# Kernel tuning notes

Measured on AMD Instinct MI355X. Metric: run time of the kernel, lower is better.

The kernel has to match this reference:

```python
import jax, jax.numpy as jnp
import numpy as np

HEADS = 8
DIM_HEAD = 64
SCALE = DIM_HEAD ** -0.5


def setup_inputs() -> dict:
    key = jax.random.key(0)
    k1, k2, k3, k4 = jax.random.split(key, 4)
    b, n, dim = 4, 1024, 512
    inner = HEADS * DIM_HEAD  # 512
    x = jax.random.normal(k1, (b, n, dim), dtype=jnp.float32)
    spd = jax.random.normal(k2, (b, HEADS, n, n), dtype=jnp.float32)
    head_keep = jnp.ones((HEADS,), dtype=jnp.float32)  # deterministic stand-in for binomial head drop
    w_qkv = jax.random.normal(k3, (dim, 3 * inner), dtype=jnp.float32) * (dim ** -0.5)
    w_out = jax.random.normal(k4, (inner, dim), dtype=jnp.float32) * (inner ** -0.5)
    b_out = jnp.zeros((dim,), dtype=jnp.float32)
    return {"x": x, "spd": spd, "head_keep": head_keep, "w_qkv": w_qkv, "w_out": w_out, "b_out": b_out}


def reference(x, spd, head_keep, w_qkv, w_out, b_out):
    b, n, dim = x.shape
    qkv = x @ w_qkv  # [b, n, 3*inner]
    q, k, v = jnp.split(qkv, 3, axis=-1)

    def to_heads(t):  # [b, n, h*d] -> [b, h, n, d]
        return t.reshape(b, n, HEADS, DIM_HEAD).transpose(0, 2, 1, 3)

    q, k, v = to_heads(q), to_heads(k), to_heads(v)
    dots = jnp.einsum('bhid,bhjd->bhij', q, k) * SCALE + spd  # [b, h, n, n]
    attn = jax.nn.softmax(dots, axis=-1)
    # random head drop + rescale: attn * mask * H / sum(keep)
    keep_sum = jnp.sum(head_keep)
    attn = attn * (head_keep[None, :, None, None] * (HEADS / keep_sum))
    out = jnp.einsum('bhij,bhjd->bhid', attn, v)  # [b, h, n, d]
    out = out.transpose(0, 2, 1, 3).reshape(b, n, HEADS * DIM_HEAD)
    return out @ w_out + b_out
```

## Files before the change

### kernel.cpp

```cpp
#include <hip/hip_runtime.h>
#include <math.h>

#define NSEQ   1024
#define HEADS  8
#define DHEAD  64
#define SCALE  0.125f
#define LOG2E  1.4426950408889634f

typedef unsigned int u32;
typedef unsigned short u16;
typedef short short8 __attribute__((ext_vector_type(8)));
typedef __bf16 bf16x2 __attribute__((ext_vector_type(2)));
typedef __bf16 bf16x8 __attribute__((ext_vector_type(8)));
typedef float f32x4  __attribute__((ext_vector_type(4)));
typedef float f32x16 __attribute__((ext_vector_type(16)));

__device__ __forceinline__ u16 f2bf(float f) {
    __bf16 h = (__bf16)f;
    return __builtin_bit_cast(u16, h);
}
__device__ __forceinline__ u32 pk2(float lo, float hi) {
    bf16x2 v; v[0] = (__bf16)lo; v[1] = (__bf16)hi;
    return __builtin_bit_cast(u32, v);
}
__device__ __forceinline__ short8 cvt8(float4 a, float4 b) {
    bf16x8 v;
    v[0] = (__bf16)a.x; v[1] = (__bf16)a.y; v[2] = (__bf16)a.z; v[3] = (__bf16)a.w;
    v[4] = (__bf16)b.x; v[5] = (__bf16)b.y; v[6] = (__bf16)b.z; v[7] = (__bf16)b.w;
    return __builtin_bit_cast(short8, v);
}
__device__ __forceinline__ float exp2_fast(float x) {
#if __has_builtin(__builtin_amdgcn_exp2f)
    return __builtin_amdgcn_exp2f(x);
#else
    return exp2f(x);
#endif
}
__device__ __forceinline__ f32x4 mfma16(short8 a, short8 b, f32x4 c) {
    return __builtin_amdgcn_mfma_f32_16x16x32_bf16(a, b, c, 0, 0, 0);
}
__device__ __forceinline__ f32x16 mfma32(short8 a, short8 b, f32x16 c) {
    return __builtin_amdgcn_mfma_f32_32x32x16_bf16(a, b, c, 0, 0, 0);
}

__global__ __launch_bounds__(256) void prep(const float* __restrict__ wqkv,
                                            const float* __restrict__ wout,
                                            u16* __restrict__ wqkvT,
                                            u16* __restrict__ woutT) {
    __shared__ float T[64][65];
    const int t = threadIdx.x;
    const int bb = blockIdx.x;
    const float* in; u16* outp; int K, N, n0, k0;
    if (bb < 192) {
        in = wqkv; outp = wqkvT; K = 512; N = 1536;
        n0 = (bb % 24) * 64; k0 = (bb / 24) * 64;
    } else {
        int bid = bb - 192;
        in = wout; outp = woutT; K = 512; N = 512;
        n0 = (bid % 8) * 64; k0 = (bid / 8) * 64;
    }
    #pragma unroll
    for (int rep = 0; rep < 4; ++rep) {
        int r = rep * 16 + (t >> 4), c = (t & 15) * 4;
        float4 v = *(const float4*)&in[(size_t)(k0 + r) * N + n0 + c];
        T[r][c + 0] = v.x; T[r][c + 1] = v.y; T[r][c + 2] = v.z; T[r][c + 3] = v.w;
    }
    __syncthreads();
    const int nl = t >> 2, kb = (t & 3) * 16;
    bf16x8 s0, s1;
    #pragma unroll
    for (int e = 0; e < 8; ++e) s0[e] = (__bf16)T[kb + e][nl];
    #pragma unroll
    for (int e = 0; e < 8; ++e) s1[e] = (__bf16)T[kb + 8 + e][nl];
    *(short8*)&outp[(size_t)(n0 + nl) * K + k0 + kb]     = __builtin_bit_cast(short8, s0);
    *(short8*)&outp[(size_t)(n0 + nl) * K + k0 + kb + 8] = __builtin_bit_cast(short8, s1);
}

__global__ __launch_bounds__(256) void gemm_qkv_mfma(const float* __restrict__ x,
                                                     const u16* __restrict__ wT,
                                                     u16* __restrict__ qb,
                                                     u16* __restrict__ kb,
                                                     u16* __restrict__ vT) {
    __shared__ u16 As[128][72];
    __shared__ u16 Bs[64][72];
    const int t = threadIdx.x, lane = t & 63, w = t >> 6;
    const int wm = w >> 1, wn = w & 1;
    const int l15 = lane & 15, l4 = lane >> 4;
    const int bid = blockIdx.x;
    const int swz = (bid & 7) * 96 + (bid >> 3);
    const int j0 = (swz % 24) * 64, i0 = (swz / 24) * 128;
    const int which = j0 / 512;
    const int b = i0 >> 10;

    f32x4 acc[8];
    #pragma unroll
    for (int i = 0; i < 8; ++i) acc[i] = (f32x4){0.f, 0.f, 0.f, 0.f};

    const int arow0 = t >> 2, c16 = (t & 3) * 16;

    float4 rax[8];
    short8 rb2[2];
    #pragma unroll
    for (int rep = 0; rep < 2; ++rep)
        #pragma unroll
        for (int q = 0; q < 4; ++q)
            rax[rep * 4 + q] = *(const float4*)&x[(size_t)(i0 + rep * 64 + arow0) * 512 + c16 + q * 4];
    #pragma unroll
    for (int q = 0; q < 2; ++q)
        rb2[q] = *(const short8*)&wT[(size_t)(j0 + arow0) * 512 + c16 + q * 8];

    for (int kt = 0; kt < 8; ++kt) {
        __syncthreads();
        #pragma unroll
        for (int rep = 0; rep < 2; ++rep) {
            *(short8*)&As[rep * 64 + arow0][c16]     = cvt8(rax[rep * 4 + 0], rax[rep * 4 + 1]);
            *(short8*)&As[rep * 64 + arow0][c16 + 8] = cvt8(rax[rep * 4 + 2], rax[rep * 4 + 3]);
        }
        *(short8*)&Bs[arow0][c16]     = rb2[0];
        *(short8*)&Bs[arow0][c16 + 8] = rb2[1];
        __syncthreads();
        if (kt < 7) {
            int k0 = (kt + 1) * 64;
            #pragma unroll
            for (int rep = 0; rep < 2; ++rep)
                #pragma unroll
                for (int q = 0; q < 4; ++q)
                    rax[rep * 4 + q] = *(const float4*)&x[(size_t)(i0 + rep * 64 + arow0) * 512 + k0 + c16 + q * 4];
            #pragma unroll
            for (int q = 0; q < 2; ++q)
                rb2[q] = *(const short8*)&wT[(size_t)(j0 + arow0) * 512 + k0 + c16 + q * 8];
        }
        #pragma unroll
        for (int ks = 0; ks < 2; ++ks) {
            if (which < 2) {
                short8 af[4], bf[2];
                #pragma unroll
                for (int m = 0; m < 4; ++m)
                    af[m] = *(const short8*)&As[wm * 64 + m * 16 + l15][ks * 32 + l4 * 8];
                #pragma unroll
                for (int n = 0; n < 2; ++n)
                    bf[n] = *(const short8*)&Bs[wn * 32 + n * 16 + l15][ks * 32 + l4 * 8];
                #pragma unroll
                for (int m = 0; m < 4; ++m)
                    #pragma unroll
                    for (int n = 0; n < 2; ++n)
                        acc[m * 2 + n] = mfma16(af[m], bf[n], acc[m * 2 + n]);
            } else {
                short8 af[2], bf[4];
                #pragma unroll
                for (int mj = 0; mj < 2; ++mj)
                    af[mj] = *(const short8*)&Bs[wn * 32 + mj * 16 + l15][ks * 32 + l4 * 8];
                #pragma unroll
                for (int ni = 0; ni < 4; ++ni)
                    bf[ni] = *(const short8*)&As[wm * 64 + ni * 16 + l15][ks * 32 + l4 * 8];
                #pragma unroll
                for (int mj = 0; mj < 2; ++mj)
                    #pragma unroll
                    for (int ni = 0; ni < 4; ++ni)
                        acc[mj * 4 + ni] = mfma16(af[mj], bf[ni], acc[mj * 4 + ni]);
            }
        }
    }

    if (which < 2) {
        u16* dst = (which == 0) ? qb : kb;
        const int h = (j0 & 511) >> 6;
        #pragma unroll
        for (int m = 0; m < 4; ++m)
            #pragma unroll
            for (int n = 0; n < 2; ++n) {
                int d = wn * 32 + n * 16 + l15;
                #pragma unroll
                for (int r = 0; r < 4; ++r) {
                    int tok = i0 + wm * 64 + m * 16 + l4 * 4 + r;
                    dst[(((size_t)(b * HEADS + h)) * NSEQ + (tok & 1023)) * DHEAD + d] =
                        f2bf(acc[m * 2 + n][r]);
                }
            }
    } else {
        const int h = (j0 - 1024) >> 6;
        #pragma unroll
        for (int mj = 0; mj < 2; ++mj)
            #pragma unroll
            for (int ni = 0; ni < 4; ++ni) {
                int tok = i0 + wm * 64 + ni * 16 + l15;
                #pragma unroll
                for (int r = 0; r < 4; ++r) {
                    int d = wn * 32 + mj * 16 + l4 * 4 + r;
                    vT[(((size_t)(b * HEADS + h)) * DHEAD + d) * NSEQ + (tok & 1023)] =
                        f2bf(acc[mj * 4 + ni][r]);
                }
            }
    }
}

__global__ __launch_bounds__(256) void attn_mfma(const u16* __restrict__ qb,
                                                 const u16* __restrict__ kb,
                                                 const u16* __restrict__ vT,
                                                 const float* __restrict__ spd,
                                                 const float* __restrict__ head_keep,
                                                 u16* __restrict__ ab) {
    __shared__ u16 Qs[128][72];
    __shared__ u16 Ks[64][72];
    __shared__ u16 Vs[64][72];
    __shared__ float Ss[128][65];

    const int t = threadIdx.x, lane = t & 63, w = t >> 6;
    const int hi = lane >> 5, li = lane & 31;
    const int bh = blockIdx.y, b = bh >> 3, h = bh & 7;
    const int i0 = blockIdx.x * 128;

    const u16* qh = qb + (size_t)bh * NSEQ * DHEAD;
    const u16* kh = kb + (size_t)bh * NSEQ * DHEAD;
    const u16* vh = vT + (size_t)bh * DHEAD * NSEQ;
    const float* sp = spd + (size_t)bh * NSEQ * NSEQ;

    #pragma unroll
    for (int rep = 0; rep < 4; ++rep) {
        int row = rep * 32 + (t >> 3), c8 = (t & 7) * 8;
        *(short8*)&Qs[row][c8] = *(const short8*)&qh[(size_t)(i0 + row) * DHEAD + c8];
    }

    float m_s = -1e30f, l_s = 0.f;
    f32x16 o0 = {}, o1 = {};
    #pragma unroll
    for (int r = 0; r < 16; ++r) { o0[r] = 0.f; o1[r] = 0.f; }

    short8 rk[2], rv[2];
    float4 rs[8];
    {
        int row = t >> 3, c8 = (t & 7) * 8;
        #pragma unroll
        for (int rep = 0; rep < 2; ++rep) {
            rk[rep] = *(const short8*)&kh[(size_t)(rep * 32 + row) * DHEAD + c8];
            rv[rep] = *(const short8*)&vh[(size_t)(rep * 32 + row) * NSEQ + c8];
        }
        #pragma unroll
        for (int rep = 0; rep < 8; ++rep) {
            int rrow = rep * 16 + (t >> 4), c = (t & 15) * 4;
            rs[rep] = *(const float4*)&sp[(size_t)(i0 + rrow) * NSEQ + c];
        }
    }

    for (int jt = 0; jt < 16; ++jt) {
        __syncthreads();
        {
            int row = t >> 3, c8 = (t & 7) * 8;
            #pragma unroll
            for (int rep = 0; rep < 2; ++rep) {
                *(short8*)&Ks[rep * 32 + row][c8] = rk[rep];
                *(short8*)&Vs[rep * 32 + row][c8] = rv[rep];
            }
            #pragma unroll
            for (int rep = 0; rep < 8; ++rep) {
                int rrow = rep * 16 + (t >> 4), c = (t & 15) * 4;
                Ss[rrow][c + 0] = rs[rep].x * LOG2E;
                Ss[rrow][c + 1] = rs[rep].y * LOG2E;
                Ss[rrow][c + 2] = rs[rep].z * LOG2E;
                Ss[rrow][c + 3] = rs[rep].w * LOG2E;
            }
        }
        __syncthreads();
        if (jt < 15) {
            int j0n = (jt + 1) * 64;
            int row = t >> 3, c8 = (t & 7) * 8;
            #pragma unroll
            for (int rep = 0; rep < 2; ++rep) {
                rk[rep] = *(const short8*)&kh[(size_t)(j0n + rep * 32 + row) * DHEAD + c8];
                rv[rep] = *(const short8*)&vh[(size_t)(rep * 32 + row) * NSEQ + j0n + c8];
            }
            #pragma unroll
            for (int rep = 0; rep < 8; ++rep) {
                int rrow = rep * 16 + (t >> 4), c = (t & 15) * 4;
                rs[rep] = *(const float4*)&sp[(size_t)(i0 + rrow) * NSEQ + j0n + c];
            }
        }

        f32x16 s2[2];
        #pragma unroll
        for (int kg = 0; kg < 2; ++kg) {
            #pragma unroll
            for (int r = 0; r < 16; ++r) s2[kg][r] = 0.f;
            #pragma unroll
            for (int ds = 0; ds < 4; ++ds) {
                short8 ak = *(const short8*)&Ks[kg * 32 + li][ds * 16 + hi * 8];
                short8 bq = *(const short8*)&Qs[w * 32 + li][ds * 16 + hi * 8];
                s2[kg] = mfma32(ak, bq, s2[kg]);
            }
        }

        float p2[32];
        #pragma unroll
        for (int kg = 0; kg < 2; ++kg)
            #pragma unroll
            for (int r = 0; r < 16; ++r) {
                int key = kg * 32 + (r & 3) + 8 * (r >> 2) + 4 * hi;
                p2[kg * 16 + r] = fmaf(s2[kg][r], SCALE * LOG2E, Ss[w * 32 + li][key]);
            }
        float m16[16];
        #pragma unroll
        for (int r = 0; r < 16; ++r) m16[r] = fmaxf(p2[r], p2[r + 16]);
        float m8v[8];
        #pragma unroll
        for (int r = 0; r < 8; ++r) m8v[r] = fmaxf(m16[r], m16[r + 8]);
        float m4v[4];
        #pragma unroll
        for (int r = 0; r < 4; ++r) m4v[r] = fmaxf(m8v[r], m8v[r + 4]);
        float pmax = fmaxf(fmaxf(m4v[0], m4v[1]), fmaxf(m4v[2], m4v[3]));
        pmax = fmaxf(pmax, __shfl_xor(pmax, 32));

        if (!__all(pmax <= m_s + 12.0f)) {
            float mnew = fmaxf(m_s, pmax);
            float fac = exp2_fast(m_s - mnew);
            m_s = mnew;
            l_s *= fac;
            #pragma unroll
            for (int r = 0; r < 16; ++r) {
                int ip = (r & 3) + 8 * (r >> 2) + 4 * hi;
                float fr = __shfl(fac, ip);
                o0[r] *= fr; o1[r] *= fr;
            }
        }

        float p[32];
        float sa0 = 0.f, sa1 = 0.f, sa2 = 0.f, sa3 = 0.f;
        #pragma unroll
        for (int r = 0; r < 32; r += 4) {
            p[r + 0] = exp2_fast(p2[r + 0] - m_s); sa0 += p[r + 0];
            p[r + 1] = exp2_fast(p2[r + 1] - m_s); sa1 += p[r + 1];
            p[r + 2] = exp2_fast(p2[r + 2] - m_s); sa2 += p[r + 2];
            p[r + 3] = exp2_fast(p2[r + 3] - m_s); sa3 += p[r + 3];
        }
        float rsum = (sa0 + sa1) + (sa2 + sa3);
        rsum += __shfl_xor(rsum, 32);
        l_s += rsum;

        short8 pf[4];
        #pragma unroll
        for (int ks = 0; ks < 4; ++ks) {
            int rb = (ks >> 1) * 16 + (ks & 1) * 8;
            u32 a0 = pk2(p[rb + 0], p[rb + 1]);
            u32 a1 = pk2(p[rb + 2], p[rb + 3]);
            u32 a2 = pk2(p[rb + 4], p[rb + 5]);
            u32 a3 = pk2(p[rb + 6], p[rb + 7]);
            u32 x0 = (u32)__shfl_xor((int)a0, 32);
            u32 x1 = (u32)__shfl_xor((int)a1, 32);
            u32 x2 = (u32)__shfl_xor((int)a2, 32);
            u32 x3 = (u32)__shfl_xor((int)a3, 32);
            union { u32 u[4]; short8 v; } c4;
            c4.u[0] = hi ? x2 : a0;
            c4.u[1] = hi ? x3 : a1;
            c4.u[2] = hi ? a2 : x0;
            c4.u[3] = hi ? a3 : x1;
            pf[ks] = c4.v;
        }

        #pragma unroll
        for (int ks = 0; ks < 4; ++ks) {
            short8 v0f = *(const short8*)&Vs[li][ks * 16 + hi * 8];
            short8 v1f = *(const short8*)&Vs[32 + li][ks * 16 + hi * 8];
            o0 = mfma32(pf[ks], v0f, o0);
            o1 = mfma32(pf[ks], v1f, o1);
        }
    }

    float ksum = 0.f;
    #pragma unroll
    for (int i = 0; i < HEADS; ++i) ksum += head_keep[i];
    const float hscale = head_keep[h] * (float)HEADS / ksum;
    const float inv = hscale / l_s;
    #pragma unroll
    for (int r = 0; r < 16; ++r) {
        int ip = (r & 3) + 8 * (r >> 2) + 4 * hi;
        float invr = __shfl(inv, ip);
        int tok = i0 + w * 32 + ip;
        size_t base = ((size_t)(b * NSEQ) + tok) * 512 + h * DHEAD;
        ab[base + li]      = f2bf(o0[r] * invr);
        ab[base + 32 + li] = f2bf(o1[r] * invr);
    }
}

__global__ __launch_bounds__(256) void gemm_out_mfma(const u16* __restrict__ abuf,
                                                     const u16* __restrict__ wT,
                                                     const float* __restrict__ bias,
                                                     float* __restrict__ out) {
    __shared__ u16 As[64][72];
    __shared__ u16 Bs[64][72];
    const int t = threadIdx.x, lane = t & 63, w = t >> 6;
    const int wm = w >> 1, wn = w & 1;
    const int l15 = lane & 15, l4 = lane >> 4;
    const int bid = blockIdx.x;
    const int swz = (bid & 7) * 64 + (bid >> 3);
    const int j0 = (swz % 8) * 64, i0 = (swz / 8) * 64;

    f32x4 acc[2][2];
    #pragma unroll
    for (int m = 0; m < 2; ++m)
        #pragma unroll
        for (int n = 0; n < 2; ++n) acc[m][n] = (f32x4){0.f, 0.f, 0.f, 0.f};

    const int row0 = t >> 2, c16 = (t & 3) * 16;
    short8 rav[2], rbv[2];
    #pragma unroll
    for (int q = 0; q < 2; ++q) {
        rav[q] = *(const short8*)&abuf[(size_t)(i0 + row0) * 512 + c16 + q * 8];
        rbv[q] = *(const short8*)&wT[(size_t)(j0 + row0) * 512 + c16 + q * 8];
    }

    for (int kt = 0; kt < 8; ++kt) {
        __syncthreads();
        #pragma unroll
        for (int q = 0; q < 2; ++q) {
            *(short8*)&As[row0][c16 + q * 8] = rav[q];
            *(short8*)&Bs[row0][c16 + q * 8] = rbv[q];
        }
        __syncthreads();
        if (kt < 7) {
            int k0 = (kt + 1) * 64;
            #pragma unroll
            for (int q = 0; q < 2; ++q) {
                rav[q] = *(const short8*)&abuf[(size_t)(i0 + row0) * 512 + k0 + c16 + q * 8];
                rbv[q] = *(const short8*)&wT[(size_t)(j0 + row0) * 512 + k0 + c16 + q * 8];
            }
        }
        #pragma unroll
        for (int ks = 0; ks < 2; ++ks) {
            short8 af[2], bf[2];
            #pragma unroll
            for (int m = 0; m < 2; ++m)
                af[m] = *(const short8*)&As[wm * 32 + m * 16 + l15][ks * 32 + l4 * 8];
            #pragma unroll
            for (int n = 0; n < 2; ++n)
                bf[n] = *(const short8*)&Bs[wn * 32 + n * 16 + l15][ks * 32 + l4 * 8];
            #pragma unroll
            for (int m = 0; m < 2; ++m)
                #pragma unroll
                for (int n = 0; n < 2; ++n)
                    acc[m][n] = mfma16(af[m], bf[n], acc[m][n]);
        }
    }

    #pragma unroll
    for (int m = 0; m < 2; ++m)
        #pragma unroll
        for (int n = 0; n < 2; ++n) {
            int col = j0 + wn * 32 + n * 16 + l15;
            float bb = bias[col];
            #pragma unroll
            for (int r = 0; r < 4; ++r) {
                int row = i0 + wm * 32 + m * 16 + l4 * 4 + r;
                out[(size_t)row * 512 + col] = acc[m][n][r] + bb;
            }
        }
}

extern "C" void kernel_launch(void* const* d_in, const int* in_sizes, int n_in,
                              void* d_out, int out_size, void* d_ws, size_t ws_size,
                              hipStream_t stream) {
    const float* x         = (const float*)d_in[0];
    const float* spd       = (const float*)d_in[1];
    const float* head_keep = (const float*)d_in[2];
    const float* w_qkv     = (const float*)d_in[3];
    const float* w_out     = (const float*)d_in[4];
    const float* b_out     = (const float*)d_in[5];
    float* out = (float*)d_out;

    char* ws = (char*)d_ws;
    u16* wqkvT  = (u16*)(ws + (4u << 20));
    u16* woutT  = (u16*)(ws + (4u << 20) + 1572864);
    u16* qb     = (u16*)(ws + (6u << 20));
    u16* kb     = (u16*)(ws + (10u << 20));
    u16* vT     = (u16*)(ws + (14u << 20));
    u16* ab     = (u16*)(ws + (18u << 20));

    prep<<<256, 256, 0, stream>>>(w_qkv, w_out, wqkvT, woutT);
    gemm_qkv_mfma<<<768, 256, 0, stream>>>(x, wqkvT, qb, kb, vT);
    attn_mfma<<<dim3(8, 32), 256, 0, stream>>>(qb, kb, vT, spd, head_keep, ab);
    gemm_out_mfma<<<512, 256, 0, stream>>>(ab, woutT, b_out, out);
}
```

Baseline: 69.36 us.

## Double-buffer K/V tiles and read spd bias directly into registers

The attention kernel now double-buffers K and V tiles in shared memory, so each iteration needs one barrier instead of two. The spd bias is loaded straight from global memory into registers in the MFMA output layout, which drops the Ss shared-memory staging buffer. The loop is unrolled by two with ping-pong register sets, and launch bounds are raised to one block minimum. Each lane now reads strided float4 segments of its own spd row, which may coalesce less well, and register pressure goes up.

```diff
diff --git a/kernel.cpp b/kernel.cpp
--- a/kernel.cpp
+++ b/kernel.cpp
@@ -194,26 +194,26 @@
     }
 }
 
-__global__ __launch_bounds__(256) void attn_mfma(const u16* __restrict__ qb,
-                                                 const u16* __restrict__ kb,
-                                                 const u16* __restrict__ vT,
-                                                 const float* __restrict__ spd,
-                                                 const float* __restrict__ head_keep,
-                                                 u16* __restrict__ ab) {
+__global__ __launch_bounds__(256, 1) void attn_mfma(const u16* __restrict__ qb,
+                                                    const u16* __restrict__ kb,
+                                                    const u16* __restrict__ vT,
+                                                    const float* __restrict__ spd,
+                                                    const float* __restrict__ head_keep,
+                                                    u16* __restrict__ ab) {
     __shared__ u16 Qs[128][72];
-    __shared__ u16 Ks[64][72];
-    __shared__ u16 Vs[64][72];
-    __shared__ float Ss[128][65];
+    __shared__ u16 Kd[2][64][72];
+    __shared__ u16 Vd[2][64][72];
 
     const int t = threadIdx.x, lane = t & 63, w = t >> 6;
     const int hi = lane >> 5, li = lane & 31;
     const int bh = blockIdx.y, b = bh >> 3, h = bh & 7;
     const int i0 = blockIdx.x * 128;
+    const int irow = i0 + w * 32 + li;
 
     const u16* qh = qb + (size_t)bh * NSEQ * DHEAD;
     const u16* kh = kb + (size_t)bh * NSEQ * DHEAD;
     const u16* vh = vT + (size_t)bh * DHEAD * NSEQ;
-    const float* sp = spd + (size_t)bh * NSEQ * NSEQ;
+    const float* sp = spd + (size_t)bh * NSEQ * NSEQ + (size_t)irow * NSEQ + hi * 4;
 
     #pragma unroll
     for (int rep = 0; rep < 4; ++rep) {
@@ -221,148 +221,138 @@
         *(short8*)&Qs[row][c8] = *(const short8*)&qh[(size_t)(i0 + row) * DHEAD + c8];
     }
 
+    const int krow = t >> 3, kc8 = (t & 7) * 8;
+
+    short8 rk[2], rv[2];
+    float4 spA[8], spB[8];
+    #pragma unroll
+    for (int rep = 0; rep < 2; ++rep) {
+        rk[rep] = *(const short8*)&kh[(size_t)(rep * 32 + krow) * DHEAD + kc8];
+        rv[rep] = *(const short8*)&vh[(size_t)(rep * 32 + krow) * NSEQ + kc8];
+    }
+    #pragma unroll
+    for (int e = 0; e < 8; ++e)
+        spA[e] = *(const float4*)&sp[(e >> 2) * 32 + (e & 3) * 8];
+    #pragma unroll
+    for (int rep = 0; rep < 2; ++rep) {
+        *(short8*)&Kd[0][rep * 32 + krow][kc8] = rk[rep];
+        *(short8*)&Vd[0][rep * 32 + krow][kc8] = rv[rep];
+    }
+    __syncthreads();
+
     float m_s = -1e30f, l_s = 0.f;
     f32x16 o0 = {}, o1 = {};
     #pragma unroll
     for (int r = 0; r < 16; ++r) { o0[r] = 0.f; o1[r] = 0.f; }
 
-    short8 rk[2], rv[2];
-    float4 rs[8];
-    {
-        int row = t >> 3, c8 = (t & 7) * 8;
-        #pragma unroll
-        for (int rep = 0; rep < 2; ++rep) {
-            rk[rep] = *(const short8*)&kh[(size_t)(rep * 32 + row) * DHEAD + c8];
-            rv[rep] = *(const short8*)&vh[(size_t)(rep * 32 + row) * NSEQ + c8];
-        }
-        #pragma unroll
-        for (int rep = 0; rep < 8; ++rep) {
-            int rrow = rep * 16 + (t >> 4), c = (t & 15) * 4;
-            rs[rep] = *(const float4*)&sp[(size_t)(i0 + rrow) * NSEQ + c];
-        }
-    }
-
-    for (int jt = 0; jt < 16; ++jt) {
-        __syncthreads();
-        {
-            int row = t >> 3, c8 = (t & 7) * 8;
-            #pragma unroll
-            for (int rep = 0; rep < 2; ++rep) {
-                *(short8*)&Ks[rep * 32 + row][c8] = rk[rep];
-                *(short8*)&Vs[rep * 32 + row][c8] = rv[rep];
-            }
-            #pragma unroll
-            for (int rep = 0; rep < 8; ++rep) {
-                int rrow = rep * 16 + (t >> 4), c = (t & 15) * 4;
-                Ss[rrow][c + 0] = rs[rep].x * LOG2E;
-                Ss[rrow][c + 1] = rs[rep].y * LOG2E;
-                Ss[rrow][c + 2] = rs[rep].z * LOG2E;
-                Ss[rrow][c + 3] = rs[rep].w * LOG2E;
-            }
-        }
-        __syncthreads();
-        if (jt < 15) {
-            int j0n = (jt + 1) * 64;
-            int row = t >> 3, c8 = (t & 7) * 8;
-            #pragma unroll
-            for (int rep = 0; rep < 2; ++rep) {
-                rk[rep] = *(const short8*)&kh[(size_t)(j0n + rep * 32 + row) * DHEAD + c8];
-                rv[rep] = *(const short8*)&vh[(size_t)(rep * 32 + row) * NSEQ + j0n + c8];
-            }
-            #pragma unroll
-            for (int rep = 0; rep < 8; ++rep) {
-                int rrow = rep * 16 + (t >> 4), c = (t & 15) * 4;
-                rs[rep] = *(const float4*)&sp[(size_t)(i0 + rrow) * NSEQ + j0n + c];
-            }
-        }
-
-        f32x16 s2[2];
-        #pragma unroll
-        for (int kg = 0; kg < 2; ++kg) {
-            #pragma unroll
-            for (int r = 0; r < 16; ++r) s2[kg][r] = 0.f;
-            #pragma unroll
-            for (int ds = 0; ds < 4; ++ds) {
-                short8 ak = *(const short8*)&Ks[kg * 32 + li][ds * 16 + hi * 8];
-                short8 bq = *(const short8*)&Qs[w * 32 + li][ds * 16 + hi * 8];
-                s2[kg] = mfma32(ak, bq, s2[kg]);
-            }
-        }
-
-        float p2[32];
-        #pragma unroll
-        for (int kg = 0; kg < 2; ++kg)
-            #pragma unroll
-            for (int r = 0; r < 16; ++r) {
-                int key = kg * 32 + (r & 3) + 8 * (r >> 2) + 4 * hi;
-                p2[kg * 16 + r] = fmaf(s2[kg][r], SCALE * LOG2E, Ss[w * 32 + li][key]);
-            }
-        float m16[16];
-        #pragma unroll
-        for (int r = 0; r < 16; ++r) m16[r] = fmaxf(p2[r], p2[r + 16]);
-        float m8v[8];
-        #pragma unroll
-        for (int r = 0; r < 8; ++r) m8v[r] = fmaxf(m16[r], m16[r + 8]);
-        float m4v[4];
-        #pragma unroll
-        for (int r = 0; r < 4; ++r) m4v[r] = fmaxf(m8v[r], m8v[r + 4]);
-        float pmax = fmaxf(fmaxf(m4v[0], m4v[1]), fmaxf(m4v[2], m4v[3]));
-        pmax = fmaxf(pmax, __shfl_xor(pmax, 32));
-
-        if (!__all(pmax <= m_s + 12.0f)) {
-            float mnew = fmaxf(m_s, pmax);
-            float fac = exp2_fast(m_s - mnew);
-            m_s = mnew;
-            l_s *= fac;
-            #pragma unroll
-            for (int r = 0; r < 16; ++r) {
-                int ip = (r & 3) + 8 * (r >> 2) + 4 * hi;
-                float fr = __shfl(fac, ip);
-                o0[r] *= fr; o1[r] *= fr;
-            }
-        }
-
-        float p[32];
-        float sa0 = 0.f, sa1 = 0.f, sa2 = 0.f, sa3 = 0.f;
-        #pragma unroll
-        for (int r = 0; r < 32; r += 4) {
-            p[r + 0] = exp2_fast(p2[r + 0] - m_s); sa0 += p[r + 0];
-            p[r + 1] = exp2_fast(p2[r + 1] - m_s); sa1 += p[r + 1];
-            p[r + 2] = exp2_fast(p2[r + 2] - m_s); sa2 += p[r + 2];
-            p[r + 3] = exp2_fast(p2[r + 3] - m_s); sa3 += p[r + 3];
-        }
-        float rsum = (sa0 + sa1) + (sa2 + sa3);
-        rsum += __shfl_xor(rsum, 32);
-        l_s += rsum;
-
-        short8 pf[4];
-        #pragma unroll
-        for (int ks = 0; ks < 4; ++ks) {
-            int rb = (ks >> 1) * 16 + (ks & 1) * 8;
-            u32 a0 = pk2(p[rb + 0], p[rb + 1]);
-            u32 a1 = pk2(p[rb + 2], p[rb + 3]);
-            u32 a2 = pk2(p[rb + 4], p[rb + 5]);
-            u32 a3 = pk2(p[rb + 6], p[rb + 7]);
-            u32 x0 = (u32)__shfl_xor((int)a0, 32);
-            u32 x1 = (u32)__shfl_xor((int)a1, 32);
-            u32 x2 = (u32)__shfl_xor((int)a2, 32);
-            u32 x3 = (u32)__shfl_xor((int)a3, 32);
-            union { u32 u[4]; short8 v; } c4;
-            c4.u[0] = hi ? x2 : a0;
-            c4.u[1] = hi ? x3 : a1;
-            c4.u[2] = hi ? a2 : x0;
-            c4.u[3] = hi ? a3 : x1;
-            pf[ks] = c4.v;
-        }
-
-        #pragma unroll
-        for (int ks = 0; ks < 4; ++ks) {
-            short8 v0f = *(const short8*)&Vs[li][ks * 16 + hi * 8];
-            short8 v1f = *(const short8*)&Vs[32 + li][ks * 16 + hi * 8];
-            o0 = mfma32(pf[ks], v0f, o0);
-            o1 = mfma32(pf[ks], v1f, o1);
-        }
-    }
+#define ATTN_STEP(JT, CUR, SPU, SPL)                                          \
+    {                                                                         \
+        const int jn_ = (JT) + 1;                                             \
+        if (jn_ < 16) {                      \
+            int j0n = jn_ * 64;                                               \
+            _Pragma("unroll")                                                 \
+            for (int rep = 0; rep < 2; ++rep) {                               \
+                rk[rep] = *(const short8*)&kh[(size_t)(j0n + rep * 32 + krow) * DHEAD + kc8]; \
+                rv[rep] = *(const short8*)&vh[(size_t)(rep * 32 + krow) * NSEQ + j0n + kc8];  \
+            }                                                                 \
+            _Pragma("unroll")                                                 \
+            for (int e = 0; e < 8; ++e)                                       \
+                SPL[e] = *(const float4*)&sp[j0n + (e >> 2) * 32 + (e & 3) * 8]; \
+        }                                                                     \
+        f32x16 s2[2];                                                         \
+        _Pragma("unroll")                                                     \
+        for (int kg = 0; kg < 2; ++kg) {                                      \
+            _Pragma("unroll")                                                 \
+            for (int r = 0; r < 16; ++r) s2[kg][r] = 0.f;                     \
+            _Pragma("unroll")                                                 \
+            for (int ds = 0; ds < 4; ++ds) {                                  \
+                short8 ak = *(const short8*)&Kd[CUR][kg * 32 + li][ds * 16 + hi * 8]; \
+                short8 bq = *(const short8*)&Qs[w * 32 + li][ds * 16 + hi * 8];       \
+                s2[kg] = mfma32(ak, bq, s2[kg]);                              \
+            }                                                                 \
+        }                                                                     \
+                          \
+        _Pragma("unroll")                                                     \
+        for (int kg = 0; kg < 2; ++kg)                                        \
+            _Pragma("unroll")                                                 \
+            for (int r = 0; r < 16; ++r)                                      \
+                s2[kg][r] = fmaf(s2[kg][r], SCALE, SPU[kg * 4 + (r >> 2)][r & 3]) * LOG2E; \
+        float mx_[8];                                                         \
+        _Pragma("unroll")                                                     \
+        for (int r = 0; r < 8; ++r)                                           \
+            mx_[r] = fmaxf(fmaxf(s2[0][r], s2[0][r + 8]),                     \
+                           fmaxf(s2[1][r], s2[1][r + 8]));                    \
+        float m4_[4];                                                         \
+        _Pragma("unroll")                                                     \
+        for (int r = 0; r < 4; ++r) m4_[r] = fmaxf(mx_[r], mx_[r + 4]);       \
+        float pmax = fmaxf(fmaxf(m4_[0], m4_[1]), fmaxf(m4_[2], m4_[3]));     \
+        pmax = fmaxf(pmax, __shfl_xor(pmax, 32));                             \
+        if (!__all(pmax <= m_s + 12.0f)) {                                    \
+            float mnew = fmaxf(m_s, pmax);                                    \
+            float fac = exp2_fast(m_s - mnew);                                \
+            m_s = mnew;                                                       \
+            l_s *= fac;                                                       \
+            _Pragma("unroll")                                                 \
+            for (int r = 0; r < 16; ++r) {                                    \
+                int ip = (r & 3) + 8 * (r >> 2) + 4 * hi;                     \
+                float fr = __shfl(fac, ip);                                   \
+                o0[r] *= fr; o1[r] *= fr;                                     \
+            }                                                                 \
+        }                                                                     \
+        float sa0 = 0.f, sa1 = 0.f, sa2 = 0.f, sa3 = 0.f;                     \
+        _Pragma("unroll")                                                     \
+        for (int kg = 0; kg < 2; ++kg)                                        \
+            _Pragma("unroll")                                                 \
+            for (int r = 0; r < 16; r += 4) {                                 \
+                s2[kg][r + 0] = exp2_fast(s2[kg][r + 0] - m_s); sa0 += s2[kg][r + 0]; \
+                s2[kg][r + 1] = exp2_fast(s2[kg][r + 1] - m_s); sa1 += s2[kg][r + 1]; \
+                s2[kg][r + 2] = exp2_fast(s2[kg][r + 2] - m_s); sa2 += s2[kg][r + 2]; \
+                s2[kg][r + 3] = exp2_fast(s2[kg][r + 3] - m_s); sa3 += s2[kg][r + 3]; \
+            }                                                                 \
+        float rsum = (sa0 + sa1) + (sa2 + sa3);                               \
+        rsum += __shfl_xor(rsum, 32);                                         \
+        l_s += rsum;                                                          \
+        short8 pf[4];                                                         \
+        _Pragma("unroll")                                                     \
+        for (int ks = 0; ks < 4; ++ks) {                                      \
+            int kg_ = ks >> 1, rb_ = (ks & 1) * 8;                            \
+            u32 a0 = pk2(s2[kg_][rb_ + 0], s2[kg_][rb_ + 1]);                 \
+            u32 a1 = pk2(s2[kg_][rb_ + 2], s2[kg_][rb_ + 3]);                 \
+            u32 a2 = pk2(s2[kg_][rb_ + 4], s2[kg_][rb_ + 5]);                 \
+            u32 a3 = pk2(s2[kg_][rb_ + 6], s2[kg_][rb_ + 7]);                 \
+            u32 x0 = (u32)__shfl_xor((int)a0, 32);                            \
+            u32 x1 = (u32)__shfl_xor((int)a1, 32);                            \
+            u32 x2 = (u32)__shfl_xor((int)a2, 32);                            \
+            u32 x3 = (u32)__shfl_xor((int)a3, 32);                            \
+            union { u32 u[4]; short8 v; } c4;                                 \
+            c4.u[0] = hi ? x2 : a0;                                           \
+            c4.u[1] = hi ? x3 : a1;                                           \
+            c4.u[2] = hi ? a2 : x0;                                           \
+            c4.u[3] = hi ? a3 : x1;                                           \
+            pf[ks] = c4.v;                                                    \
+        }                                                                     \
+        _Pragma("unroll")                                                     \
+        for (int ks = 0; ks < 4; ++ks) {                                      \
+            short8 v0f = *(const short8*)&Vd[CUR][li][ks * 16 + hi * 8];      \
+            short8 v1f = *(const short8*)&Vd[CUR][32 + li][ks * 16 + hi * 8]; \
+            o0 = mfma32(pf[ks], v0f, o0);                                     \
+            o1 = mfma32(pf[ks], v1f, o1);                                     \
+        }                                                                     \
+        if (jn_ < 16) {                  \
+            _Pragma("unroll")                                                 \
+            for (int rep = 0; rep < 2; ++rep) {                               \
+                *(short8*)&Kd[(CUR) ^ 1][rep * 32 + krow][kc8] = rk[rep];     \
+                *(short8*)&Vd[(CUR) ^ 1][rep * 32 + krow][kc8] = rv[rep];     \
+            }                                                                 \
+            __syncthreads();                                                  \
+        }                                                                     \
+    }
+
+    for (int jt2 = 0; jt2 < 16; jt2 += 2) {
+        ATTN_STEP(jt2,     0, spA, spB)
+        ATTN_STEP(jt2 + 1, 1, spB, spA)
+    }
+#undef ATTN_STEP
 
     float ksum = 0.f;
     #pragma unroll
```

Measured after the change: 73.76 us. +6.3%, slower.

## Halve attention query tile to 64 rows with 2 waves and swizzled block order

Applied to the files above, without the earlier changes.

The attention kernel now processes 64 query rows per block using 128 threads (2 waves) instead of 128 rows with 256 threads. This doubles the grid to 512 blocks for better CU coverage on the 256-CU part. It adds a block-index swizzle that spreads consecutive blocks across different (batch, head) pairs, and computes softmax in place in the MFMA accumulators to cut register use. The cost is that each K/V tile is loaded by twice as many blocks, and launch_bounds(128,1) may limit occupancy hints.

```diff
diff --git a/kernel.cpp b/kernel.cpp
--- a/kernel.cpp
+++ b/kernel.cpp
@@ -194,86 +194,81 @@
     }
 }
 
-__global__ __launch_bounds__(256) void attn_mfma(const u16* __restrict__ qb,
-                                                 const u16* __restrict__ kb,
-                                                 const u16* __restrict__ vT,
-                                                 const float* __restrict__ spd,
-                                                 const float* __restrict__ head_keep,
-                                                 u16* __restrict__ ab) {
-    __shared__ u16 Qs[128][72];
+__global__ __launch_bounds__(128, 1) void attn_mfma(const u16* __restrict__ qb,
+                                                    const u16* __restrict__ kb,
+                                                    const u16* __restrict__ vT,
+                                                    const float* __restrict__ spd,
+                                                    const float* __restrict__ head_keep,
+                                                    u16* __restrict__ ab) {
+    __shared__ u16 Qs[64][72];
     __shared__ u16 Ks[64][72];
     __shared__ u16 Vs[64][72];
-    __shared__ float Ss[128][65];
+    __shared__ float Ss[64][65];
 
     const int t = threadIdx.x, lane = t & 63, w = t >> 6;
     const int hi = lane >> 5, li = lane & 31;
-    const int bh = blockIdx.y, b = bh >> 3, h = bh & 7;
-    const int i0 = blockIdx.x * 128;
+    const int bid = blockIdx.x;
+    const int swz = (bid & 7) * 64 + (bid >> 3);
+    const int bh = swz >> 4, it = swz & 15;
+    const int b = bh >> 3, h = bh & 7;
+    const int i0 = it * 64;
 
     const u16* qh = qb + (size_t)bh * NSEQ * DHEAD;
     const u16* kh = kb + (size_t)bh * NSEQ * DHEAD;
     const u16* vh = vT + (size_t)bh * DHEAD * NSEQ;
     const float* sp = spd + (size_t)bh * NSEQ * NSEQ;
 
-    #pragma unroll
-    for (int rep = 0; rep < 4; ++rep) {
-        int row = rep * 32 + (t >> 3), c8 = (t & 7) * 8;
-        *(short8*)&Qs[row][c8] = *(const short8*)&qh[(size_t)(i0 + row) * DHEAD + c8];
-    }
+    const int qrow = t >> 3, qc8 = (t & 7) * 8;
+    #pragma unroll
+    for (int rep = 0; rep < 4; ++rep)
+        *(short8*)&Qs[rep * 16 + qrow][qc8] =
+            *(const short8*)&qh[(size_t)(i0 + rep * 16 + qrow) * DHEAD + qc8];
 
     float m_s = -1e30f, l_s = 0.f;
     f32x16 o0 = {}, o1 = {};
     #pragma unroll
     for (int r = 0; r < 16; ++r) { o0[r] = 0.f; o1[r] = 0.f; }
 
-    short8 rk[2], rv[2];
+    short8 rk[4], rv[4];
     float4 rs[8];
-    {
-        int row = t >> 3, c8 = (t & 7) * 8;
-        #pragma unroll
-        for (int rep = 0; rep < 2; ++rep) {
-            rk[rep] = *(const short8*)&kh[(size_t)(rep * 32 + row) * DHEAD + c8];
-            rv[rep] = *(const short8*)&vh[(size_t)(rep * 32 + row) * NSEQ + c8];
-        }
-        #pragma unroll
-        for (int rep = 0; rep < 8; ++rep) {
-            int rrow = rep * 16 + (t >> 4), c = (t & 15) * 4;
-            rs[rep] = *(const float4*)&sp[(size_t)(i0 + rrow) * NSEQ + c];
-        }
-    }
+    const int srow = t >> 4, sc = (t & 15) * 4;
+    #pragma unroll
+    for (int rep = 0; rep < 4; ++rep) {
+        rk[rep] = *(const short8*)&kh[(size_t)(rep * 16 + qrow) * DHEAD + qc8];
+        rv[rep] = *(const short8*)&vh[(size_t)(rep * 16 + qrow) * NSEQ + qc8];
+    }
+    #pragma unroll
+    for (int rep = 0; rep < 8; ++rep)
+        rs[rep] = *(const float4*)&sp[(size_t)(i0 + rep * 8 + srow) * NSEQ + sc];
 
     for (int jt = 0; jt < 16; ++jt) {
         __syncthreads();
         {
-            int row = t >> 3, c8 = (t & 7) * 8;
-            #pragma unroll
-            for (int rep = 0; rep < 2; ++rep) {
-                *(short8*)&Ks[rep * 32 + row][c8] = rk[rep];
-                *(short8*)&Vs[rep * 32 + row][c8] = rv[rep];
+            #pragma unroll
+            for (int rep = 0; rep < 4; ++rep) {
+                *(short8*)&Ks[rep * 16 + qrow][qc8] = rk[rep];
+                *(short8*)&Vs[rep * 16 + qrow][qc8] = rv[rep];
             }
             #pragma unroll
             for (int rep = 0; rep < 8; ++rep) {
-                int rrow = rep * 16 + (t >> 4), c = (t & 15) * 4;
-                Ss[rrow][c + 0] = rs[rep].x * LOG2E;
-                Ss[rrow][c + 1] = rs[rep].y * LOG2E;
-                Ss[rrow][c + 2] = rs[rep].z * LOG2E;
-                Ss[rrow][c + 3] = rs[rep].w * LOG2E;
+                int rrow = rep * 8 + srow;
+                Ss[rrow][sc + 0] = rs[rep].x * LOG2E;
+                Ss[rrow][sc + 1] = rs[rep].y * LOG2E;
+                Ss[rrow][sc + 2] = rs[rep].z * LOG2E;
+                Ss[rrow][sc + 3] = rs[rep].w * LOG2E;
             }
         }
         __syncthreads();
         if (jt < 15) {
             int j0n = (jt + 1) * 64;
-            int row = t >> 3, c8 = (t & 7) * 8;
-            #pragma unroll
-            for (int rep = 0; rep < 2; ++rep) {
-                rk[rep] = *(const short8*)&kh[(size_t)(j0n + rep * 32 + row) * DHEAD + c8];
-                rv[rep] = *(const short8*)&vh[(size_t)(rep * 32 + row) * NSEQ + j0n + c8];
-            }
-            #pragma unroll
-            for (int rep = 0; rep < 8; ++rep) {
-                int rrow = rep * 16 + (t >> 4), c = (t & 15) * 4;
-                rs[rep] = *(const float4*)&sp[(size_t)(i0 + rrow) * NSEQ + j0n + c];
-            }
+            #pragma unroll
+            for (int rep = 0; rep < 4; ++rep) {
+                rk[rep] = *(const short8*)&kh[(size_t)(j0n + rep * 16 + qrow) * DHEAD + qc8];
+                rv[rep] = *(const short8*)&vh[(size_t)(rep * 16 + qrow) * NSEQ + j0n + qc8];
+            }
+            #pragma unroll
+            for (int rep = 0; rep < 8; ++rep)
+                rs[rep] = *(const float4*)&sp[(size_t)(i0 + rep * 8 + srow) * NSEQ + j0n + sc];
         }
 
         f32x16 s2[2];
@@ -289,24 +284,21 @@
             }
         }
 
-        float p2[32];
         #pragma unroll
         for (int kg = 0; kg < 2; ++kg)
             #pragma unroll
             for (int r = 0; r < 16; ++r) {
                 int key = kg * 32 + (r & 3) + 8 * (r >> 2) + 4 * hi;
-                p2[kg * 16 + r] = fmaf(s2[kg][r], SCALE * LOG2E, Ss[w * 32 + li][key]);
-            }
-        float m16[16];
-        #pragma unroll
-        for (int r = 0; r < 16; ++r) m16[r] = fmaxf(p2[r], p2[r + 16]);
-        float m8v[8];
-        #pragma unroll
-        for (int r = 0; r < 8; ++r) m8v[r] = fmaxf(m16[r], m16[r + 8]);
-        float m4v[4];
-        #pragma unroll
-        for (int r = 0; r < 4; ++r) m4v[r] = fmaxf(m8v[r], m8v[r + 4]);
-        float pmax = fmaxf(fmaxf(m4v[0], m4v[1]), fmaxf(m4v[2], m4v[3]));
+                s2[kg][r] = fmaf(s2[kg][r], SCALE * LOG2E, Ss[w * 32 + li][key]);
+            }
+        float mx_[8];
+        #pragma unroll
+        for (int r = 0; r < 8; ++r)
+            mx_[r] = fmaxf(fmaxf(s2[0][r], s2[0][r + 8]), fmaxf(s2[1][r], s2[1][r + 8]));
+        float m4_[4];
+        #pragma unroll
+        for (int r = 0; r < 4; ++r) m4_[r] = fmaxf(mx_[r], mx_[r + 4]);
+        float pmax = fmaxf(fmaxf(m4_[0], m4_[1]), fmaxf(m4_[2], m4_[3]));
         pmax = fmaxf(pmax, __shfl_xor(pmax, 32));
 
         if (!__all(pmax <= m_s + 12.0f)) {
@@ -322,15 +314,16 @@
             }
         }
 
-        float p[32];
         float sa0 = 0.f, sa1 = 0.f, sa2 = 0.f, sa3 = 0.f;
         #pragma unroll
-        for (int r = 0; r < 32; r += 4) {
-            p[r + 0] = exp2_fast(p2[r + 0] - m_s); sa0 += p[r + 0];
-            p[r + 1] = exp2_fast(p2[r + 1] - m_s); sa1 += p[r + 1];
-            p[r + 2] = exp2_fast(p2[r + 2] - m_s); sa2 += p[r + 2];
-            p[r + 3] = exp2_fast(p2[r + 3] - m_s); sa3 += p[r + 3];
-        }
+        for (int kg = 0; kg < 2; ++kg)
+            #pragma unroll
+            for (int r = 0; r < 16; r += 4) {
+                s2[kg][r + 0] = exp2_fast(s2[kg][r + 0] - m_s); sa0 += s2[kg][r + 0];
+                s2[kg][r + 1] = exp2_fast(s2[kg][r + 1] - m_s); sa1 += s2[kg][r + 1];
+                s2[kg][r + 2] = exp2_fast(s2[kg][r + 2] - m_s); sa2 += s2[kg][r + 2];
+                s2[kg][r + 3] = exp2_fast(s2[kg][r + 3] - m_s); sa3 += s2[kg][r + 3];
+            }
         float rsum = (sa0 + sa1) + (sa2 + sa3);
         rsum += __shfl_xor(rsum, 32);
         l_s += rsum;
@@ -338,11 +331,11 @@
         short8 pf[4];
         #pragma unroll
         for (int ks = 0; ks < 4; ++ks) {
-            int rb = (ks >> 1) * 16 + (ks & 1) * 8;
-            u32 a0 = pk2(p[rb + 0], p[rb + 1]);
-            u32 a1 = pk2(p[rb + 2], p[rb + 3]);
-            u32 a2 = pk2(p[rb + 4], p[rb + 5]);
-            u32 a3 = pk2(p[rb + 6], p[rb + 7]);
+            int kg_ = ks >> 1, rb_ = (ks & 1) * 8;
+            u32 a0 = pk2(s2[kg_][rb_ + 0], s2[kg_][rb_ + 1]);
+            u32 a1 = pk2(s2[kg_][rb_ + 2], s2[kg_][rb_ + 3]);
+            u32 a2 = pk2(s2[kg_][rb_ + 4], s2[kg_][rb_ + 5]);
+            u32 a3 = pk2(s2[kg_][rb_ + 6], s2[kg_][rb_ + 7]);
             u32 x0 = (u32)__shfl_xor((int)a0, 32);
             u32 x1 = (u32)__shfl_xor((int)a1, 32);
             u32 x2 = (u32)__shfl_xor((int)a2, 32);
@@ -475,6 +468,6 @@
 
     prep<<<256, 256, 0, stream>>>(w_qkv, w_out, wqkvT, woutT);
     gemm_qkv_mfma<<<768, 256, 0, stream>>>(x, wqkvT, qb, kb, vT);
-    attn_mfma<<<dim3(8, 32), 256, 0, stream>>>(qb, kb, vT, spd, head_keep, ab);
+    attn_mfma<<<512, 128, 0, stream>>>(qb, kb, vT, spd, head_keep, ab);
     gemm_out_mfma<<<512, 256, 0, stream>>>(ab, woutT, b_out, out);
 }
```

Result: slower. 71.09 us (+2.5%).
